# Kernel optimization log

Hardware: AMD Instinct MI355X
Metric: run time of the kernel (lower is better)

Reference implementation:

```python
import jax, jax.numpy as jnp
import numpy as np

BN_EPS = 1e-5

# Binary activation with hardtanh STE semantics (forward: sign)
@jax.custom_vjp
def binary_act(x):
    return jnp.sign(x)

def _ba_fwd(x):
    return jnp.sign(x), x

def _ba_bwd(x, g):
    return (jnp.where(jnp.abs(x) > 1.0, 0.0, g),)

binary_act.defvjp(_ba_fwd, _ba_bwd)

# Binary weight quantizer (forward: sign, backward: identity STE)
@jax.custom_vjp
def binary_w(x):
    return jnp.sign(x)

def _bw_fwd(x):
    return jnp.sign(x), None

def _bw_bwd(_, g):
    return (g,)

binary_w.defvjp(_bw_fwd, _bw_bwd)


def setup_inputs() -> dict:
    key = jax.random.key(0)
    k1, k2, k3 = jax.random.split(key, 3)
    B, C_in, H, W_sp = 32, 256, 56, 56
    C_out, KH, KW = 256, 3, 3
    x = jax.random.normal(k1, (B, C_in, H, W_sp), dtype=jnp.float32)
    weight = jax.random.normal(k2, (C_out, C_in, KH, KW), dtype=jnp.float32) * 0.05
    bias = jax.random.normal(k3, (C_out,), dtype=jnp.float32) * 0.01
    gamma = jnp.ones((C_out,), dtype=jnp.float32)
    beta = jnp.zeros((C_out,), dtype=jnp.float32)
    return {"x": x, "weight": weight, "bias": bias, "gamma": gamma, "beta": beta}


def reference(x, weight, bias, gamma, beta):
    # --- activation binarization (A=2): sign ---
    xb = binary_act(x)
    # --- weight binarization (W=2): mean-center over in-channel dim, clamp, sign * alpha ---
    wc = weight - jnp.mean(weight, axis=1, keepdims=True)
    wc = jnp.clip(wc, -1.0, 1.0)
    alpha = jnp.mean(jnp.abs(wc), axis=(1, 2, 3), keepdims=True)  # per-output-channel scale
    wq = binary_w(wc) * alpha
    # --- conv2d, stride 1, padding 1 ---
    y = jax.lax.conv_general_dilated(
        xb, wq, window_strides=(1, 1), padding=((1, 1), (1, 1)),
        dimension_numbers=("NCHW", "OIHW", "NCHW"))
    y = y + bias[None, :, None, None]
    # --- BatchNorm2d (training-mode batch statistics, biased variance) ---
    mu = jnp.mean(y, axis=(0, 2, 3), keepdims=True)
    var = jnp.var(y, axis=(0, 2, 3), keepdims=True)
    y = (y - mu) * jax.lax.rsqrt(var + BN_EPS)
    y = y * gamma[None, :, None, None] + beta[None, :, None, None]
    # --- last_relu=1 ---
    y = jax.nn.relu(y)
    # --- last_bin=1 (A=2 -> binary activation) ---
    y = binary_act(y)
    return y
```

## Files before the change

kernel.cpp:

```cpp
#include <hip/hip_runtime.h>

typedef unsigned long long u64;
typedef int i32x4 __attribute__((ext_vector_type(4)));
typedef int i32x16 __attribute__((ext_vector_type(16)));

#define N_SP 3136
#define C_IN 256
#define C_OUT 256
#define BATCH 32
#define XROW 64
#define XPLANE (58 * XROW * 256)
#define XSIZE ((size_t)BATCH * XPLANE)

__global__ __launch_bounds__(256) void prep_weights(const float* __restrict__ w,
                                                    char* __restrict__ A_pack,
                                                    double* __restrict__ alpha) {
    const int o = blockIdx.x;
    const int i = threadIdx.x;
    const int lane = i & 63, wvid = i >> 6;
    __shared__ double part[4][9];
    __shared__ double part2[4];

    float wv[9];
    const float* wp = w + ((size_t)o * C_IN + i) * 9;
#pragma unroll
    for (int t = 0; t < 9; ++t) wv[t] = wp[t];

#pragma unroll
    for (int t = 0; t < 9; ++t) {
        double v = (double)wv[t];
#pragma unroll
        for (int off = 32; off > 0; off >>= 1) v += __shfl_down(v, off);
        if (lane == 0) part[wvid][t] = v;
    }
    __syncthreads();

    double asum = 0.0;
#pragma unroll
    for (int t = 0; t < 9; ++t) {
        double mean = (part[0][t] + part[1][t] + part[2][t] + part[3][t]) * (1.0 / 256.0);
        double wc = (double)wv[t] - mean;
        int idx16 = ((t * 8 + (i >> 5)) * 8 + (o >> 5)) * 64 + (((i >> 4) & 1) << 5) + (o & 31);
        A_pack[(size_t)idx16 * 16 + (i & 15)] = (char)(wc > 0.0 ? 1 : -1);
        double aw = fabs(wc);
        if (aw > 1.0) aw = 1.0;
        asum += aw;
    }
#pragma unroll
    for (int off = 32; off > 0; off >>= 1) asum += __shfl_down(asum, off);
    if (lane == 0) part2[wvid] = asum;
    __syncthreads();
    if (i == 0)
        alpha[o] = (part2[0] + part2[1] + part2[2] + part2[3]) * (1.0 / 2304.0);
}

__global__ __launch_bounds__(256) void zero_xsignT(i32x4* __restrict__ p) {
    p[(size_t)blockIdx.x * 256 + threadIdx.x] = (i32x4){0, 0, 0, 0};
}

__global__ __launch_bounds__(256) void sign_transpose(const float* __restrict__ x,
                                                      char* __restrict__ xsT) {
    const int sp0 = blockIdx.x * 64;
    const int b = blockIdx.y;
    const int lane = threadIdx.x & 63;
    const int wv = threadIdx.x >> 6;
    __shared__ char tile[64 * 272];

    const float* xp = x + ((size_t)(b * 256 + (wv << 6))) * N_SP + sp0 + lane;
#pragma unroll
    for (int q = 0; q < 4; ++q) {
        unsigned d[4];
#pragma unroll
        for (int dd = 0; dd < 4; ++dd) {
            unsigned v = 0;
#pragma unroll
            for (int kk = 0; kk < 4; ++kk) {
                int ci_l = (q << 4) + (dd << 2) + kk;
                float xv = xp[(size_t)ci_l * N_SP];
                v |= (unsigned)(xv > 0.0f ? 0x01u : 0xFFu) << (8 * kk);
            }
            d[dd] = v;
        }
        *(i32x4*)(tile + lane * 272 + (wv << 6) + (q << 4)) =
            (i32x4){(int)d[0], (int)d[1], (int)d[2], (int)d[3]};
    }
    __syncthreads();

    const int t = threadIdx.x;
#pragma unroll
    for (int j = 0; j < 4; ++j) {
        int sp_loc = (j << 4) + (t >> 4);
        int ci0 = (t & 15) << 4;
        i32x4 v = *(const i32x4*)(tile + sp_loc * 272 + ci0);
        int spg = sp0 + sp_loc;
        int h = spg / 56, w = spg - h * 56;
        size_t dst = (((size_t)(b * 58 + h + 1) << 6) + (w + 1)) * 256 + ci0;
        *(i32x4*)(xsT + dst) = v;
    }
}

__global__ __launch_bounds__(256, 2) void conv_mfma(const char* __restrict__ xsT,
                                                    const char* __restrict__ A_pack,
                                                    float* __restrict__ out) {
    const int tid = threadIdx.x;
    const int lane = tid & 63;
    const int wv = tid >> 6;
    const int l31 = lane & 31, l5 = lane >> 5;
    const int r = blockIdx.x;
    const int b = r / 56, h = r - (r / 56) * 56;

    __shared__ char slab[3 * 66 * 272];

    {
        const char* src = xsT + ((size_t)(b * 58 + h) << 6) * 256;
        for (int c = tid; c < 3 * 64 * 16; c += 256) {
            int dh = c >> 10, rem = c & 1023, wp = rem >> 4, c16 = (rem & 15) << 4;
            *(i32x4*)(slab + (dh * 66 + wp) * 272 + c16) =
                *(const i32x4*)(src + (size_t)dh * (XROW * 256) + wp * 256 + c16);
        }
        for (int c = tid; c < 96; c += 256) {
            int dh = c >> 5, wp = 64 + ((c >> 4) & 1), c16 = (c & 15) << 4;
            *(i32x4*)(slab + (dh * 66 + wp) * 272 + c16) = (i32x4){0, 0, 0, 0};
        }
    }
    __syncthreads();

    i32x16 acc00 = {0}, acc01 = {0}, acc10 = {0}, acc11 = {0};

#pragma unroll
    for (int tap = 0; tap < 9; ++tap) {
        const int dh = tap / 3, dw = tap % 3;
        i32x4 af[8][2];
#pragma unroll
        for (int cib = 0; cib < 8; ++cib)
#pragma unroll
            for (int a = 0; a < 2; ++a)
                af[cib][a] = *(const i32x4*)(A_pack +
                    ((size_t)(((tap * 8 + cib) * 8 + wv * 2 + a) * 64 + lane) << 4));
        const char* bp0 = slab + (dh * 66 + l31 + dw) * 272 + l5 * 16;
        const char* bp1 = bp0 + 32 * 272;
#pragma unroll
        for (int cib = 0; cib < 8; ++cib) {
            i32x4 bf0 = *(const i32x4*)(bp0 + cib * 32);
            i32x4 bf1 = *(const i32x4*)(bp1 + cib * 32);
            acc00 = __builtin_amdgcn_mfma_i32_32x32x32_i8(af[cib][0], bf0, acc00, 0, 0, 0);
            acc01 = __builtin_amdgcn_mfma_i32_32x32x32_i8(af[cib][0], bf1, acc01, 0, 0, 0);
            acc10 = __builtin_amdgcn_mfma_i32_32x32x32_i8(af[cib][1], bf0, acc10, 0, 0, 0);
            acc11 = __builtin_amdgcn_mfma_i32_32x32x32_i8(af[cib][1], bf1, acc11, 0, 0, 0);
        }
    }

    float* ob = out + ((size_t)(b * 256 + wv * 64)) * N_SP + h * 56;
#pragma unroll
    for (int a = 0; a < 2; ++a)
#pragma unroll
        for (int nh = 0; nh < 2; ++nh) {
            const i32x16 A_ = (a == 0) ? (nh == 0 ? acc00 : acc01)
                                       : (nh == 0 ? acc10 : acc11);
            const int w = nh * 32 + l31;
            if (w < 56) {
#pragma unroll
                for (int reg = 0; reg < 16; ++reg) {
                    int row = (reg & 3) + 8 * (reg >> 2) + 4 * l5;
                    ob[(size_t)(a * 32 + row) * N_SP + w] = (float)A_[reg];
                }
            }
        }
}

__global__ __launch_bounds__(256) void stats_reduce(const float* __restrict__ out,
                                                    u64* __restrict__ stats) {
    const int c = blockIdx.x;
    const int t = threadIdx.x;
    long long s1 = 0;
    u64 s2 = 0;
    for (int i = t; i < BATCH * 784; i += 256) {
        int b = i / 784, q = i - b * 784;
        float4 v = ((const float4*)out)[(size_t)(b * 256 + c) * 784 + q];
        int x0 = (int)v.x, x1 = (int)v.y, x2 = (int)v.z, x3 = (int)v.w;
        s1 += x0 + x1 + x2 + x3;
        s2 += (u64)((long long)x0 * x0 + (long long)x1 * x1 +
                    (long long)x2 * x2 + (long long)x3 * x3);
    }
#pragma unroll
    for (int off = 32; off > 0; off >>= 1) {
        s1 += __shfl_down(s1, off);
        s2 += __shfl_down(s2, off);
    }
    __shared__ long long p1[4];
    __shared__ u64 p2[4];
    if ((t & 63) == 0) { p1[t >> 6] = s1; p2[t >> 6] = s2; }
    __syncthreads();
    if (t == 0) {
        stats[c] = (u64)(p1[0] + p1[1] + p1[2] + p1[3]);
        stats[C_OUT + c] = p2[0] + p2[1] + p2[2] + p2[3];
    }
}

__global__ void make_consts(const u64* __restrict__ stats,
                            const double* __restrict__ alpha,
                            const float* __restrict__ gamma,
                            const float* __restrict__ beta,
                            double* __restrict__ AB) {
    const int c = threadIdx.x;
    const double N = (double)(BATCH * N_SP);
    double s1 = (double)(long long)stats[c];
    double s2 = (double)(long long)stats[C_OUT + c];
    double mu = s1 / N;
    double var = s2 / N - mu * mu;
    double a = alpha[c];
    double vy = a * a * var;
    double scale = (double)gamma[c] / sqrt(vy + 1e-5);
    double A = a * scale;
    double B = (double)beta[c] - A * mu;
    AB[c] = A;
    AB[C_OUT + c] = B;
}

__global__ __launch_bounds__(256) void finalize(float* __restrict__ out,
                                                const double* __restrict__ AB) {
    const unsigned i4 = blockIdx.x * 256 + threadIdx.x;
    const unsigned e = i4 << 2;
    const int c = (int)((e / N_SP) & (C_OUT - 1));
    const double A = AB[c];
    const double B = AB[C_OUT + c];
    float4 v = ((float4*)out)[i4];
    v.x = (A * (double)v.x + B) > 0.0 ? 1.0f : 0.0f;
    v.y = (A * (double)v.y + B) > 0.0 ? 1.0f : 0.0f;
    v.z = (A * (double)v.z + B) > 0.0 ? 1.0f : 0.0f;
    v.w = (A * (double)v.w + B) > 0.0 ? 1.0f : 0.0f;
    ((float4*)out)[i4] = v;
}

extern "C" void kernel_launch(void* const* d_in, const int* in_sizes, int n_in,
                              void* d_out, int out_size, void* d_ws, size_t ws_size,
                              hipStream_t stream) {
    const float* x      = (const float*)d_in[0];
    const float* weight = (const float*)d_in[1];
    const float* bias   = (const float*)d_in[2];   (void)bias;
    const float* gamma  = (const float*)d_in[3];
    const float* beta   = (const float*)d_in[4];
    float* out = (float*)d_out;

    char* ws = (char*)d_ws;
    u64*    stats = (u64*)(ws);
    double* alpha = (double*)(ws + 4096);
    double* AB    = (double*)(ws + 8192);
    char*   A_pack = (char*)(ws + 16384);
    char*   xsT   = (char*)(ws + (1 << 20));

    prep_weights<<<C_OUT, 256, 0, stream>>>(weight, A_pack, alpha);
    zero_xsignT<<<(int)(XSIZE / 16 / 256), 256, 0, stream>>>((i32x4*)xsT);
    sign_transpose<<<dim3(49, BATCH), 256, 0, stream>>>(x, xsT);
    conv_mfma<<<BATCH * 56, 256, 0, stream>>>(xsT, A_pack, out);
    stats_reduce<<<C_OUT, 256, 0, stream>>>(out, stats);
    make_consts<<<1, C_OUT, 0, stream>>>(stats, alpha, gamma, beta, AB);
    finalize<<<(out_size / 4) / 256, 256, 0, stream>>>(out, AB);
}
```

Baseline: 358.7 us.

## Compute two output rows per conv block, zero only borders, split stats reduction

The conv kernel now computes two output rows per block, loading a 4-row input slab and reusing each weight fragment across both rows. This halves the weight fetches per output and cuts the redundant slab loads, at the cost of twice as many accumulator registers and a larger shared-memory footprint. The padded-input zeroing now writes only the border cells instead of the whole buffer. The BN stats reduction is split across 8 batch slices with 64-bit atomic adds into a stats buffer that prep_weights zeroes, which gives more parallel blocks.

```diff
diff --git a/kernel.cpp b/kernel.cpp
--- a/kernel.cpp
+++ b/kernel.cpp
@@ -14,10 +14,12 @@
 
 __global__ __launch_bounds__(256) void prep_weights(const float* __restrict__ w,
                                                     char* __restrict__ A_pack,
-                                                    double* __restrict__ alpha) {
+                                                    double* __restrict__ alpha,
+                                                    u64* __restrict__ stats) {
     const int o = blockIdx.x;
     const int i = threadIdx.x;
     const int lane = i & 63, wvid = i >> 6;
+    if (o == 0) { stats[i] = 0ull; stats[256 + i] = 0ull; }
     __shared__ double part[4][9];
     __shared__ double part2[4];
 
@@ -54,8 +56,24 @@
         alpha[o] = (part2[0] + part2[1] + part2[2] + part2[3]) * (1.0 / 2304.0);
 }
 
-__global__ __launch_bounds__(256) void zero_xsignT(i32x4* __restrict__ p) {
-    p[(size_t)blockIdx.x * 256 + threadIdx.x] = (i32x4){0, 0, 0, 0};
+__global__ __launch_bounds__(256) void zero_borders(char* __restrict__ xsT) {
+    const int tid = blockIdx.x * 256 + threadIdx.x;
+    const int b = tid / 9216;
+    const int r = tid - b * 9216;
+    int hp, wp, c16;
+    if (r < 2048) {
+        hp = (r >> 10) * 57;
+        wp = (r >> 4) & 63;
+        c16 = (r & 15) << 4;
+    } else {
+        int r2 = r - 2048;
+        hp = 1 + (r2 >> 7);
+        int q = r2 & 127;
+        int wi = q >> 4;
+        wp = (wi == 0) ? 0 : 56 + wi;
+        c16 = (q & 15) << 4;
+    }
+    *(i32x4*)(xsT + (((size_t)(b * 58 + hp) << 6) + wp) * 256 + c16) = (i32x4){0, 0, 0, 0};
 }
 
 __global__ __launch_bounds__(256) void sign_transpose(const float* __restrict__ x,
@@ -106,64 +124,71 @@
     const int lane = tid & 63;
     const int wv = tid >> 6;
     const int l31 = lane & 31, l5 = lane >> 5;
-    const int r = blockIdx.x;
-    const int b = r / 56, h = r - (r / 56) * 56;
-
-    __shared__ char slab[3 * 66 * 272];
+    const int blk = blockIdx.x;
+    const int b = blk / 28;
+    const int h0 = (blk - b * 28) * 2;
+
+    __shared__ char slab[4 * 66 * 272];
 
     {
-        const char* src = xsT + ((size_t)(b * 58 + h) << 6) * 256;
-        for (int c = tid; c < 3 * 64 * 16; c += 256) {
+        const char* src = xsT + ((size_t)(b * 58 + h0) << 6) * 256;
+        for (int c = tid; c < 4 * 64 * 16; c += 256) {
             int dh = c >> 10, rem = c & 1023, wp = rem >> 4, c16 = (rem & 15) << 4;
             *(i32x4*)(slab + (dh * 66 + wp) * 272 + c16) =
                 *(const i32x4*)(src + (size_t)dh * (XROW * 256) + wp * 256 + c16);
         }
-        for (int c = tid; c < 96; c += 256) {
+        for (int c = tid; c < 128; c += 256) {
             int dh = c >> 5, wp = 64 + ((c >> 4) & 1), c16 = (c & 15) << 4;
             *(i32x4*)(slab + (dh * 66 + wp) * 272 + c16) = (i32x4){0, 0, 0, 0};
         }
     }
     __syncthreads();
 
-    i32x16 acc00 = {0}, acc01 = {0}, acc10 = {0}, acc11 = {0};
+    i32x16 acc[2][2][2] = {};
 
 #pragma unroll
     for (int tap = 0; tap < 9; ++tap) {
         const int dh = tap / 3, dw = tap % 3;
-        i32x4 af[8][2];
-#pragma unroll
-        for (int cib = 0; cib < 8; ++cib)
+#pragma unroll
+        for (int cib = 0; cib < 8; ++cib) {
+            i32x4 af[2];
 #pragma unroll
             for (int a = 0; a < 2; ++a)
-                af[cib][a] = *(const i32x4*)(A_pack +
+                af[a] = *(const i32x4*)(A_pack +
                     ((size_t)(((tap * 8 + cib) * 8 + wv * 2 + a) * 64 + lane) << 4));
-        const char* bp0 = slab + (dh * 66 + l31 + dw) * 272 + l5 * 16;
-        const char* bp1 = bp0 + 32 * 272;
-#pragma unroll
-        for (int cib = 0; cib < 8; ++cib) {
-            i32x4 bf0 = *(const i32x4*)(bp0 + cib * 32);
-            i32x4 bf1 = *(const i32x4*)(bp1 + cib * 32);
-            acc00 = __builtin_amdgcn_mfma_i32_32x32x32_i8(af[cib][0], bf0, acc00, 0, 0, 0);
-            acc01 = __builtin_amdgcn_mfma_i32_32x32x32_i8(af[cib][0], bf1, acc01, 0, 0, 0);
-            acc10 = __builtin_amdgcn_mfma_i32_32x32x32_i8(af[cib][1], bf0, acc10, 0, 0, 0);
-            acc11 = __builtin_amdgcn_mfma_i32_32x32x32_i8(af[cib][1], bf1, acc11, 0, 0, 0);
-        }
-    }
-
-    float* ob = out + ((size_t)(b * 256 + wv * 64)) * N_SP + h * 56;
+            i32x4 bf[2][2];
+#pragma unroll
+            for (int nh = 0; nh < 2; ++nh)
+#pragma unroll
+                for (int row = 0; row < 2; ++row)
+                    bf[nh][row] = *(const i32x4*)(slab +
+                        ((dh + row) * 66 + (nh * 32 + l31) + dw) * 272 + l5 * 16 + cib * 32);
+#pragma unroll
+            for (int a = 0; a < 2; ++a)
+#pragma unroll
+                for (int nh = 0; nh < 2; ++nh)
+#pragma unroll
+                    for (int row = 0; row < 2; ++row)
+                        acc[a][nh][row] = __builtin_amdgcn_mfma_i32_32x32x32_i8(
+                            af[a], bf[nh][row], acc[a][nh][row], 0, 0, 0);
+        }
+    }
+
+    float* ob = out + ((size_t)(b * 256 + wv * 64)) * N_SP + h0 * 56;
 #pragma unroll
     for (int a = 0; a < 2; ++a)
 #pragma unroll
         for (int nh = 0; nh < 2; ++nh) {
-            const i32x16 A_ = (a == 0) ? (nh == 0 ? acc00 : acc01)
-                                       : (nh == 0 ? acc10 : acc11);
             const int w = nh * 32 + l31;
             if (w < 56) {
 #pragma unroll
-                for (int reg = 0; reg < 16; ++reg) {
-                    int row = (reg & 3) + 8 * (reg >> 2) + 4 * l5;
-                    ob[(size_t)(a * 32 + row) * N_SP + w] = (float)A_[reg];
-                }
+                for (int row = 0; row < 2; ++row)
+#pragma unroll
+                    for (int reg = 0; reg < 16; ++reg) {
+                        int corow = (reg & 3) + 8 * (reg >> 2) + 4 * l5;
+                        ob[(size_t)(a * 32 + corow) * N_SP + row * 56 + w] =
+                            (float)acc[a][nh][row][reg];
+                    }
             }
         }
 }
@@ -171,11 +196,13 @@
 __global__ __launch_bounds__(256) void stats_reduce(const float* __restrict__ out,
                                                     u64* __restrict__ stats) {
     const int c = blockIdx.x;
+    const int sl = blockIdx.y;
     const int t = threadIdx.x;
     long long s1 = 0;
     u64 s2 = 0;
-    for (int i = t; i < BATCH * 784; i += 256) {
-        int b = i / 784, q = i - b * 784;
+    for (int i = t; i < 4 * 784; i += 256) {
+        int bl = i / 784, q = i - bl * 784;
+        int b = sl * 4 + bl;
         float4 v = ((const float4*)out)[(size_t)(b * 256 + c) * 784 + q];
         int x0 = (int)v.x, x1 = (int)v.y, x2 = (int)v.z, x3 = (int)v.w;
         s1 += x0 + x1 + x2 + x3;
@@ -192,8 +219,8 @@
     if ((t & 63) == 0) { p1[t >> 6] = s1; p2[t >> 6] = s2; }
     __syncthreads();
     if (t == 0) {
-        stats[c] = (u64)(p1[0] + p1[1] + p1[2] + p1[3]);
-        stats[C_OUT + c] = p2[0] + p2[1] + p2[2] + p2[3];
+        atomicAdd(&stats[c], (u64)(p1[0] + p1[1] + p1[2] + p1[3]));
+        atomicAdd(&stats[C_OUT + c], p2[0] + p2[1] + p2[2] + p2[3]);
     }
 }
 
@@ -249,11 +276,11 @@
     char*   A_pack = (char*)(ws + 16384);
     char*   xsT   = (char*)(ws + (1 << 20));
 
-    prep_weights<<<C_OUT, 256, 0, stream>>>(weight, A_pack, alpha);
-    zero_xsignT<<<(int)(XSIZE / 16 / 256), 256, 0, stream>>>((i32x4*)xsT);
+    prep_weights<<<C_OUT, 256, 0, stream>>>(weight, A_pack, alpha, stats);
+    zero_borders<<<1152, 256, 0, stream>>>(xsT);
     sign_transpose<<<dim3(49, BATCH), 256, 0, stream>>>(x, xsT);
-    conv_mfma<<<BATCH * 56, 256, 0, stream>>>(xsT, A_pack, out);
-    stats_reduce<<<C_OUT, 256, 0, stream>>>(out, stats);
+    conv_mfma<<<BATCH * 28, 256, 0, stream>>>(xsT, A_pack, out);
+    stats_reduce<<<dim3(C_OUT, 8), 256, 0, stream>>>(out, stats);
     make_consts<<<1, C_OUT, 0, stream>>>(stats, alpha, gamma, beta, AB);
     finalize<<<(out_size / 4) / 256, 256, 0, stream>>>(out, AB);
 }
```

Measured after the change: 357.4 us. Within noise of the previous version (-0.4%).
